# Kernel tuning notes

Measured on AMD Instinct MI355X. Metric: run time of the kernel, lower is better.

The kernel has to match this reference:

```python
import jax, jax.numpy as jnp
import numpy as np
import math

D = 768      # n_embd
NH = 12      # n_head
L = 4        # n_layer
E = 8        # num_experts
K = 2        # top_k
V = 50257    # vocab
H = 4 * D    # ffn hidden
MOE_LAYERS = (1, 3)


def _ln(x, g, b):
    m = x.mean(-1, keepdims=True)
    v = ((x - m) ** 2).mean(-1, keepdims=True)
    return (x - m) * jax.lax.rsqrt(v + 1e-5) * g + b


def setup_inputs() -> dict:
    key = jax.random.key(0)
    ks = iter(jax.random.split(key, 32))
    s = 0.02

    def rnd(shape):
        return jax.random.normal(next(ks), shape, dtype=jnp.float32) * s

    inp = {
        "x": jax.random.randint(next(ks), (2, 512), 0, V),
        "emb": rnd((V, D)),                       # tied embedding / output projection
        "wqkv": rnd((L, 3 * D, D)), "bqkv": jnp.zeros((L, 3 * D)),
        "wo": rnd((L, D, D)), "bo": jnp.zeros((L, D)),
        "ln1g": jnp.ones((L, D)), "ln1b": jnp.zeros((L, D)),
        "ln2g": jnp.ones((L, D)), "ln2b": jnp.zeros((L, D)),
        "sw1": rnd((2, H, D)), "sb1": jnp.zeros((2, H)),   # dense FFN layers (0, 2)
        "sw2": rnd((2, D, H)), "sb2": jnp.zeros((2, D)),
        "gw": rnd((2, E, D)),                              # router weights (layers 1, 3)
        "mw1": rnd((2, E, H, D)), "mb1": jnp.zeros((2, E, H)),
        "mw2": rnd((2, E, D, H)), "mb2": jnp.zeros((2, E, D)),
        "lnfg": jnp.ones((D,)), "lnfb": jnp.zeros((D,)),
    }
    return inp


def reference(x, emb, wqkv, bqkv, wo, bo, ln1g, ln1b, ln2g, ln2b,
              sw1, sb1, sw2, sb2, gw, mw1, mb1, mw2, mb2, lnfg, lnfb):
    b, t = x.shape
    dh = D // NH

    h = emb[x]  # [b,t,d]
    # sinusoidal positional encoding
    pos = jnp.arange(t, dtype=jnp.float32)[:, None]
    div = jnp.exp(jnp.arange(0, D, 2, dtype=jnp.float32) * (-math.log(10000.0) / D))
    pe = jnp.stack([jnp.sin(pos * div), jnp.cos(pos * div)], axis=-1).reshape(t, D)
    h = h + pe[None]

    # causal mask: query i cannot attend to key j > i
    neg = jnp.asarray(-jnp.inf, dtype=h.dtype)
    mask = jnp.where(jnp.arange(t)[None, :] > jnp.arange(t)[:, None], neg, 0.0)

    std_i = 0
    moe_i = 0
    for i in range(L):
        # pre-norm self-attention
        xn = _ln(h, ln1g[i], ln1b[i])
        qkv = xn @ wqkv[i].T + bqkv[i]          # [b,t,3d]
        q, k, v = jnp.split(qkv, 3, axis=-1)

        def heads(z):
            return z.reshape(b, t, NH, dh).transpose(0, 2, 1, 3)  # [b,nh,t,dh]

        q, k, v = heads(q), heads(k), heads(v)
        sc = jnp.einsum('bhqd,bhkd->bhqk', q, k) / math.sqrt(dh) + mask
        a = jax.nn.softmax(sc, axis=-1)
        o = jnp.einsum('bhqk,bhkd->bhqd', a, v).transpose(0, 2, 1, 3).reshape(b, t, D)
        h = h + o @ wo[i].T + bo[i]

        # pre-norm FFN (dense or MoE)
        xn = _ln(h, ln2g[i], ln2b[i])
        if i in MOE_LAYERS:
            T = b * t
            xf = xn.reshape(T, D)
            gl = xf @ gw[moe_i].T                      # router logits [T,E]
            probs = jax.nn.softmax(gl, axis=-1)
            topv, topi = jax.lax.top_k(probs, K)       # [T,K]
            w = topv / topv.sum(-1, keepdims=True)     # renormalized top-k gates
            cw = jnp.zeros_like(probs).at[jnp.arange(T)[:, None], topi].set(w)  # [T,E]
            he = jax.nn.gelu(jnp.einsum('td,ehd->teh', xf, mw1[moe_i]) + mb1[moe_i],
                             approximate=False)        # [T,E,H]
            ye = jnp.einsum('teh,edh->ted', he, mw2[moe_i]) + mb2[moe_i]        # [T,E,D]
            ff = jnp.einsum('ted,te->td', ye, cw).reshape(b, t, D)
            moe_i += 1
        else:
            ff = jax.nn.gelu(xn @ sw1[std_i].T + sb1[std_i], approximate=False) @ sw2[std_i].T + sb2[std_i]
            std_i += 1
        h = h + ff

    h = _ln(h, lnfg, lnfb)
    logits = h @ emb.T  # tied output projection, [b,t,V]
    return logits
```

## Files before the change

kernel.cpp:

```cpp
#include <hip/hip_runtime.h>
#include <hip/hip_bf16.h>
#include <cstdint>
#include <cstddef>

#define Dm   768
#define NHm  12
#define Lm   4
#define Em   8
#define Vm   50257
#define Hm   3072
#define Tm   512
#define Bm   2
#define NT   (Bm*Tm)
#define NAS  (NT*2)

typedef float f32x4 __attribute__((ext_vector_type(4)));
typedef short bf16x8 __attribute__((ext_vector_type(8)));

__device__ __forceinline__ float gelu_exact(float x) {
    return 0.5f * x * (1.0f + erff(x * 0.70710678118654752440f));
}

__device__ __forceinline__ unsigned short f2bf(float f) {
    __hip_bfloat16 h = __float2bfloat16(f);
// ... 19 lines not shown
    }
}

__global__ __launch_bounds__(256) void embed_kernel(const int* __restrict__ x,
                                                    const float* __restrict__ emb,
                                                    float* __restrict__ h) {
    int g = blockIdx.x;
    int tid = threadIdx.x;
    int tok = x[g];
    int pos = g % Tm;
    const float* erow = emb + (size_t)tok * Dm;
    for (int d = tid; d < Dm; d += 256) {
        int i2 = (d >> 1) * 2;
        float div = expf(-logf(10000.0f) * (float)i2 / (float)Dm);
        float a = (float)pos * div;
        float pe = (d & 1) ? cosf(a) : sinf(a);
        h[(size_t)g * Dm + d] = erow[d] + pe;
    }
}

__global__ __launch_bounds__(256) void ln_kernel(const float* __restrict__ in,
                                                 const float* __restrict__ g,
                                                 const float* __restrict__ b,
                                                 float* __restrict__ out) {
    int t = blockIdx.x, tid = threadIdx.x;
    const float* x = in + (size_t)t * Dm;
    float v0 = x[tid], v1 = x[tid + 256], v2 = x[tid + 512];
    __shared__ float red[256];
    red[tid] = v0 + v1 + v2;
    __syncthreads();
    for (int off = 128; off > 0; off >>= 1) {
        if (tid < off) red[tid] += red[tid + off];
        __syncthreads();
    }
    float mean = red[0] * (1.0f / Dm);
    __syncthreads();
    float d0 = v0 - mean, d1 = v1 - mean, d2 = v2 - mean;
    red[tid] = d0 * d0 + d1 * d1 + d2 * d2;
    __syncthreads();
    for (int off = 128; off > 0; off >>= 1) {
        if (tid < off) red[tid] += red[tid + off];
        __syncthreads();
    }
    float inv = rsqrtf(red[0] * (1.0f / Dm) + 1e-5f);
    float* o = out + (size_t)t * Dm;
    o[tid]       = d0 * inv * g[tid]       + b[tid];
    o[tid + 256] = d1 * inv * g[tid + 256] + b[tid + 256];
    o[tid + 512] = d2 * inv * g[tid + 512] + b[tid + 512];
}

#define MB 128
#define NB 128
#define KB 32
#define LDT 40

__device__ __forceinline__ void stage_tile(unsigned short* lds, const float* src,
                                           bool valid, int srow, int shalf) {
    union { unsigned short s[8]; uint4 v; } p0, p1;
    if (valid) {
        const float4* s4 = reinterpret_cast<const float4*>(src);
        #pragma unroll
        for (int q = 0; q < 4; ++q) {
            float4 f = s4[q];
            float vv[4] = {f.x, f.y, f.z, f.w};
            #pragma unroll
            for (int j = 0; j < 4; ++j) {
                int idx = q * 4 + j;
                unsigned short hb = f2bf(vv[j]);
                if (idx < 8) p0.s[idx] = hb; else p1.s[idx - 8] = hb;
            }
        }
// ... 15 lines not shown
        #pragma unroll
        for (int q = 0; q < 4; ++q) {
            float4 f = s4[q];
            float vv[4] = {f.x, f.y, f.z, f.w};
            #pragma unroll
            for (int j = 0; j < 4; ++j) {
                int idx = q * 4 + j;
                unsigned short hb = f2bf(vv[j]);
                unsigned short lb = f2bf(vv[j] - bf2f_bits(hb));
                if (idx < 8) { h0.s[idx] = hb; l0.s[idx] = lb; }
                else         { h1.s[idx - 8] = hb; l1.s[idx - 8] = lb; }
            }
        }
    } else {
        h0.v = make_uint4(0,0,0,0); h1.v = make_uint4(0,0,0,0);
        l0.v = make_uint4(0,0,0,0); l1.v = make_uint4(0,0,0,0);
    }
    uint4* dh = reinterpret_cast<uint4*>(&lds_hi[srow * LDT + shalf * 16]);
    dh[0] = h0.v; dh[1] = h1.v;
    uint4* dl = reinterpret_cast<uint4*>(&lds_lo[srow * LDT + shalf * 16]);
    dl[0] = l0.v; dl[1] = l1.v;
}

__global__ __launch_bounds__(256) void mfma_gemm_bf(const unsigned short* __restrict__ A,
                                                    const unsigned short* __restrict__ B,
                                                    const float* __restrict__ bias,
                                                    float* __restrict__ C,
                                                    int M, int N, int K) {
    __shared__ __align__(16) unsigned short SMEM[2 * MB * LDT];
    unsigned short* As = SMEM;
    unsigned short* Bs = SMEM + MB * LDT;
    int tid = threadIdx.x;
    int nt_m = M / MB;
    int total = gridDim.x;
    int bid = blockIdx.x;
    int swz = bid;
    if ((total & 7) == 0) {
        int chunk = total >> 3;
        swz = (bid & 7) * chunk + (bid >> 3);
    }
    int bm = (swz % nt_m) * MB;
    int bn = (swz / nt_m) * NB;
    int srow = tid >> 1, shalf = tid & 1;
    int lane = tid & 63, w = tid >> 6;
    int wr = w >> 1, wc = w & 1;
    int r0 = (lane >> 4) * 4, c0 = lane & 15;
    int kb = (lane >> 4) * 8;

    bool bval = (bn + srow) < N;
// ... 35 lines not shown
        #pragma unroll
        for (int m = 0; m < 4; ++m)
            #pragma unroll
            for (int n = 0; n < 4; ++n)
                acc[m][n] = __builtin_amdgcn_mfma_f32_16x16x32_bf16(af[m], bf[n], acc[m][n], 0, 0, 0);
        __syncthreads();
    }

    float* Ct = reinterpret_cast<float*>(SMEM);
    float* cw = Ct + w * 1024;
    #pragma unroll
    for (int m = 0; m < 4; ++m) {
        #pragma unroll
        for (int n = 0; n < 4; ++n)
            #pragma unroll
            for (int r = 0; r < 4; ++r)
                cw[(r0 + r) * 64 + n * 16 + c0] = acc[m][n][r];
        #pragma unroll
        for (int ch = 0; ch < 4; ++ch) {
            f32x4 vv = *reinterpret_cast<const f32x4*>(&cw[ch * 256 + lane * 4]);
            int rg = bm + wr * 64 + m * 16 + ch * 4 + (lane >> 4);
            int cg = bn + wc * 64 + (lane & 15) * 4;
            if (cg + 3 < N) {
                if (bias) {
                    vv[0] += bias[cg]; vv[1] += bias[cg + 1];
                    vv[2] += bias[cg + 2]; vv[3] += bias[cg + 3];
                }
                *reinterpret_cast<f32x4*>(&C[(size_t)rg * N + cg]) = vv;
            } else {
                #pragma unroll
                for (int e = 0; e < 4; ++e)
                    if (cg + e < N)
                        C[(size_t)rg * N + cg + e] = vv[e] + (bias ? bias[cg + e] : 0.f);
            }
        }
    }
}

template<int ACT, int RES>
__global__ __launch_bounds__(256) void mfma_gemm(const float* __restrict__ A,
                                                 const float* __restrict__ B,
                                                 const float* __restrict__ bias,
                                                 const float* __restrict__ res,
                                                 float* __restrict__ C,
                                                 int M, int N, int K) {
    __shared__ __align__(16) unsigned short As[MB * LDT];
    __shared__ __align__(16) unsigned short Bs[NB * LDT];
    int tid = threadIdx.x;
    int bm = blockIdx.y * MB, bn = blockIdx.x * NB;
    int srow = tid >> 1, shalf = tid & 1;
    int lane = tid & 63, w = tid >> 6;
    int wr = w >> 1, wc = w & 1;
    int r0 = (lane >> 4) * 4, c0 = lane & 15;
    int kb = (lane >> 4) * 8;

    f32x4 acc[4][4] = {};

    for (int kk = 0; kk < K; kk += KB) {
        stage_tile(As, A + (size_t)(bm + srow) * K + kk + shalf * 16, true, srow, shalf);
        bool bval = (bn + srow) < N;
        stage_tile(Bs, B + (size_t)(bn + srow) * K + kk + shalf * 16, bval, srow, shalf);
        __syncthreads();
        bf16x8 af[4], bf[4];
        #pragma unroll
        for (int m = 0; m < 4; ++m)
            af[m] = *reinterpret_cast<const bf16x8*>(&As[(wr * 64 + m * 16 + c0) * LDT + kb]);
        #pragma unroll
        for (int n = 0; n < 4; ++n)
            bf[n] = *reinterpret_cast<const bf16x8*>(&Bs[(wc * 64 + n * 16 + c0) * LDT + kb]);
        #pragma unroll
        for (int m = 0; m < 4; ++m)
            #pragma unroll
            for (int n = 0; n < 4; ++n)
                acc[m][n] = __builtin_amdgcn_mfma_f32_16x16x32_bf16(af[m], bf[n], acc[m][n], 0, 0, 0);
        __syncthreads();
    }

    #pragma unroll
    for (int n = 0; n < 4; ++n) {
        int col = bn + wc * 64 + n * 16 + c0;
        if (col < N) {
            float bv = bias ? bias[col] : 0.f;
            #pragma unroll
            for (int m = 0; m < 4; ++m) {
                #pragma unroll
                for (int r = 0; r < 4; ++r) {
                    int row = bm + wr * 64 + m * 16 + r0 + r;
                    float v = acc[m][n][r] + bv;
                    if (RES) v += res[(size_t)row * N + col];
                    if (ACT == 1) v = gelu_exact(v);
                    C[(size_t)row * N + col] = v;
                }
            }
        }
    }
}

__global__ __launch_bounds__(256) void mfma_gemm_sp_part(const float* __restrict__ A,
                                                         const float* __restrict__ B,
                                                         float* __restrict__ part,
                                                         int M, int N, int K, int KSPLIT) {
    __shared__ __align__(16) unsigned short SMEM[4 * MB * LDT];
    unsigned short* Ah = SMEM;
    unsigned short* Al = SMEM + MB * LDT;
    unsigned short* Bh = SMEM + 2 * MB * LDT;
    unsigned short* Bl = SMEM + 3 * MB * LDT;
    int tid = threadIdx.x;
    int bm = blockIdx.y * MB, bn = blockIdx.x * NB;
    int kc = blockIdx.z;
    int chunk = K / KSPLIT;
    int kbeg = kc * chunk;
    int srow = tid >> 1, shalf = tid & 1;
    int lane = tid & 63, w = tid >> 6;
    int wr = w >> 1, wc = w & 1;
    int r0 = (lane >> 4) * 4, c0 = lane & 15;
    int kb = (lane >> 4) * 8;

    f32x4 acc[4][4] = {};

    for (int kk = kbeg; kk < kbeg + chunk; kk += KB) {
        stage_tile_split(Ah, Al, A + (size_t)(bm + srow) * K + kk + shalf * 16, true, srow, shalf);
        stage_tile_split(Bh, Bl, B + (size_t)(bn + srow) * K + kk + shalf * 16, true, srow, shalf);
        __syncthreads();
        bf16x8 ah[4], al[4], bh[4], bl[4];
        #pragma unroll
        for (int m = 0; m < 4; ++m) {
            int o = (wr * 64 + m * 16 + c0) * LDT + kb;
            ah[m] = *reinterpret_cast<const bf16x8*>(&Ah[o]);
            al[m] = *reinterpret_cast<const bf16x8*>(&Al[o]);
        }
        #pragma unroll
        for (int n = 0; n < 4; ++n) {
            int o = (wc * 64 + n * 16 + c0) * LDT + kb;
            bh[n] = *reinterpret_cast<const bf16x8*>(&Bh[o]);
            bl[n] = *reinterpret_cast<const bf16x8*>(&Bl[o]);
        }
        #pragma unroll
        for (int m = 0; m < 4; ++m)
            #pragma unroll
            for (int n = 0; n < 4; ++n) {
                acc[m][n] = __builtin_amdgcn_mfma_f32_16x16x32_bf16(al[m], bh[n], acc[m][n], 0, 0, 0);
                acc[m][n] = __builtin_amdgcn_mfma_f32_16x16x32_bf16(ah[m], bl[n], acc[m][n], 0, 0, 0);
                acc[m][n] = __builtin_amdgcn_mfma_f32_16x16x32_bf16(ah[m], bh[n], acc[m][n], 0, 0, 0);
            }
        __syncthreads();
    }

    float* Ct = reinterpret_cast<float*>(SMEM);
    float* cw = Ct + w * 1024;
    float* P = part + (size_t)kc * M * N;
    #pragma unroll
    for (int m = 0; m < 4; ++m) {
        #pragma unroll
        for (int n = 0; n < 4; ++n)
            #pragma unroll
            for (int r = 0; r < 4; ++r)
                cw[(r0 + r) * 64 + n * 16 + c0] = acc[m][n][r];
        #pragma unroll
        for (int ch = 0; ch < 4; ++ch) {
            f32x4 vv = *reinterpret_cast<const f32x4*>(&cw[ch * 256 + lane * 4]);
            int rg = bm + wr * 64 + m * 16 + ch * 4 + (lane >> 4);
            int cg = bn + wc * 64 + (lane & 15) * 4;
            *reinterpret_cast<f32x4*>(&P[(size_t)rg * N + cg]) = vv;
        }
    }
}

template<int ACT>
__global__ __launch_bounds__(256) void reduce_dense(const float* __restrict__ part,
                                                    const float* __restrict__ bias,
                                                    float* __restrict__ C,
                                                    long MN, int N, int KSPLIT) {
    long stride = (long)gridDim.x * 256 * 4;
    for (long i = ((long)blockIdx.x * 256 + threadIdx.x) * 4; i < MN; i += stride) {
        float4 v = *reinterpret_cast<const float4*>(part + i);
        for (int kc = 1; kc < KSPLIT; ++kc) {
            float4 p = *reinterpret_cast<const float4*>(part + (size_t)kc * MN + i);
            v.x += p.x; v.y += p.y; v.z += p.z; v.w += p.w;
        }
        int col = (int)(i % N);
        float4 b = *reinterpret_cast<const float4*>(bias + col);
        v.x += b.x; v.y += b.y; v.z += b.z; v.w += b.w;
        if (ACT == 1) {
            v.x = gelu_exact(v.x); v.y = gelu_exact(v.y);
            v.z = gelu_exact(v.z); v.w = gelu_exact(v.w);
        }
        *reinterpret_cast<float4*>(C + i) = v;
    }
}

__global__ __launch_bounds__(256) void reduce_ln(const float* __restrict__ part,
                                                 const float* __restrict__ bias,
                                                 float* __restrict__ h,
                                                 const float* __restrict__ g,
                                                 const float* __restrict__ b,
                                                 float* __restrict__ xn,
                                                 int KSPLIT) {
    const long MN = (long)NT * Dm;
    int t = blockIdx.x, tid = threadIdx.x;
    float v[3];
    #pragma unroll
    for (int j = 0; j < 3; ++j) {
        int col = tid + j * 256;
        long idx = (long)t * Dm + col;
        float s = part[idx];
        for (int kc = 1; kc < KSPLIT; ++kc) s += part[(size_t)kc * MN + idx];
        s += bias[col] + h[idx];
        h[idx] = s;
        v[j] = s;
    }
    __shared__ float red[256];
    red[tid] = v[0] + v[1] + v[2];
    __syncthreads();
    for (int off = 128; off > 0; off >>= 1) {
        if (tid < off) red[tid] += red[tid + off];
        __syncthreads();
    }
    float mean = red[0] * (1.0f / Dm);
    __syncthreads();
    float d0 = v[0] - mean, d1 = v[1] - mean, d2 = v[2] - mean;
    red[tid] = d0 * d0 + d1 * d1 + d2 * d2;
    __syncthreads();
    for (int off = 128; off > 0; off >>= 1) {
        if (tid < off) red[tid] += red[tid + off];
        __syncthreads();
    }
    float inv = rsqrtf(red[0] * (1.0f / Dm) + 1e-5f);
    float* o = xn + (size_t)t * Dm;
    o[tid]       = d0 * inv * g[tid]       + b[tid];
    o[tid + 256] = d1 * inv * g[tid + 256] + b[tid + 256];
    o[tid + 512] = d2 * inv * g[tid + 512] + b[tid + 512];
}

__global__ __launch_bounds__(256) void combine_ln(float* __restrict__ h,
                                                  const float* __restrict__ ye,
                                                  const float* __restrict__ g,
                                                  const float* __restrict__ b,
                                                  float* __restrict__ xn) {
    int t = blockIdx.x, tid = threadIdx.x;
    float v[3];
    #pragma unroll
    for (int j = 0; j < 3; ++j) {
        int col = tid + j * 256;
        long idx = (long)t * Dm + col;
        float s = h[idx] + ye[(size_t)(t * 2) * Dm + col] + ye[(size_t)(t * 2 + 1) * Dm + col];
        h[idx] = s;
        v[j] = s;
    }
    __shared__ float red[256];
    red[tid] = v[0] + v[1] + v[2];
    __syncthreads();
    for (int off = 128; off > 0; off >>= 1) {
        if (tid < off) red[tid] += red[tid + off];
        __syncthreads();
    }
    float mean = red[0] * (1.0f / Dm);
    __syncthreads();
    float d0 = v[0] - mean, d1 = v[1] - mean, d2 = v[2] - mean;
    red[tid] = d0 * d0 + d1 * d1 + d2 * d2;
    __syncthreads();
    for (int off = 128; off > 0; off >>= 1) {
        if (tid < off) red[tid] += red[tid + off];
        __syncthreads();
    }
    float inv = rsqrtf(red[0] * (1.0f / Dm) + 1e-5f);
    float* o = xn + (size_t)t * Dm;
    o[tid]       = d0 * inv * g[tid]       + b[tid];
    o[tid + 256] = d1 * inv * g[tid + 256] + b[tid + 256];
    o[tid + 512] = d2 * inv * g[tid + 512] + b[tid + 512];
}

#define LDA 72
__device__ __forceinline__ void stage16a(unsigned short* dh, unsigned short* dl,
                                         const float* src) {
    union { unsigned short s[8]; uint4 v; } h0, h1, l0, l1;
    const float4* s4 = reinterpret_cast<const float4*>(src);
    #pragma unroll
    for (int q = 0; q < 4; ++q) {
        float4 f = s4[q];
        float vv[4] = {f.x, f.y, f.z, f.w};
        #pragma unroll
        for (int j = 0; j < 4; ++j) {
            int idx = q * 4 + j;
            unsigned short hb = f2bf(vv[j]);
            unsigned short lb = f2bf(vv[j] - bf2f_bits(hb));
            if (idx < 8) { h0.s[idx] = hb; l0.s[idx] = lb; }
            else         { h1.s[idx - 8] = hb; l1.s[idx - 8] = lb; }
        }
    }
    reinterpret_cast<uint4*>(dh)[0] = h0.v; reinterpret_cast<uint4*>(dh)[1] = h1.v;
    reinterpret_cast<uint4*>(dl)[0] = l0.v; reinterpret_cast<uint4*>(dl)[1] = l1.v;
}

__global__ __launch_bounds__(256) void attn_flash(const float* __restrict__ qkv,
                                                  float* __restrict__ o_out) {
    int qt = blockIdx.x;
    int bh = blockIdx.y;
    int b = bh / NHm, hh = bh % NHm;
    const int g0 = b * Tm;
    const int hoff = hh * 64;
    int tid = threadIdx.x;
    int lane = tid & 63, w = tid >> 6;
    int c0 = lane & 15, hi4 = lane >> 4;
    int kb = hi4 * 8;

    __shared__ __align__(16) unsigned short Qh[64 * LDA], Ql[64 * LDA];
    __shared__ __align__(16) unsigned short Kh[64 * LDA], Kl[64 * LDA];
    __shared__ __align__(16) unsigned short Vh[64 * LDA], Vl[64 * LDA];
    __shared__ __align__(16) unsigned short Ph[4][16 * LDA], Pl[4][16 * LDA];

    {
        int srow = tid >> 2, q = tid & 3;
        stage16a(&Qh[srow * LDA + q * 16], &Ql[srow * LDA + q * 16],
                 qkv + (size_t)(g0 + qt * 64 + srow) * (3 * Dm) + hoff + q * 16);
    }
    __syncthreads();

    f32x4 acc_o[4] = {};
// ... 97 lines not shown
        for (int kk2 = 0; kk2 < 64; kk2 += 32) {
            bf16x8 pah = *reinterpret_cast<const bf16x8*>(&Ph[w][c0 * LDA + kk2 + kb]);
            bf16x8 pal = *reinterpret_cast<const bf16x8*>(&Pl[w][c0 * LDA + kk2 + kb]);
            #pragma unroll
            for (int n = 0; n < 4; ++n) {
                bf16x8 vbh = *reinterpret_cast<const bf16x8*>(&Vh[(n * 16 + c0) * LDA + kk2 + kb]);
                bf16x8 vbl = *reinterpret_cast<const bf16x8*>(&Vl[(n * 16 + c0) * LDA + kk2 + kb]);
                acc_o[n] = __builtin_amdgcn_mfma_f32_16x16x32_bf16(pal, vbh, acc_o[n], 0, 0, 0);
                acc_o[n] = __builtin_amdgcn_mfma_f32_16x16x32_bf16(pah, vbl, acc_o[n], 0, 0, 0);
                acc_o[n] = __builtin_amdgcn_mfma_f32_16x16x32_bf16(pah, vbh, acc_o[n], 0, 0, 0);
            }
        }
        __syncthreads();
    }

    float inv[4];
    #pragma unroll
    for (int r = 0; r < 4; ++r) inv[r] = 1.0f / l_r[r];
    #pragma unroll
    for (int n = 0; n < 4; ++n)
        #pragma unroll
        for (int r = 0; r < 4; ++r) {
            int row = g0 + qt * 64 + w * 16 + hi4 * 4 + r;
            o_out[(size_t)row * Dm + hoff + n * 16 + c0] = acc_o[n][r] * inv[r];
        }
}

__global__ __launch_bounds__(256) void router_kernel(const float* __restrict__ xn,
                                                     const float* __restrict__ gw,
                                                     int* __restrict__ topi,
                                                     float* __restrict__ topw) {
    int t = blockIdx.x * 4 + (threadIdx.x >> 6);
    int lane = threadIdx.x & 63;
    const float4* x4 = reinterpret_cast<const float4*>(xn + (size_t)t * Dm);
    float4 xv[3];
    #pragma unroll
    for (int i = 0; i < 3; ++i) xv[i] = x4[lane + i * 64];

    float l[Em];
    #pragma unroll
    for (int e = 0; e < Em; ++e) {
        const float4* w4 = reinterpret_cast<const float4*>(gw + (size_t)e * Dm);
        float dot = 0.f;
        #pragma unroll
        for (int i = 0; i < 3; ++i) {
            float4 wv = w4[lane + i * 64];
            dot += xv[i].x * wv.x + xv[i].y * wv.y + xv[i].z * wv.z + xv[i].w * wv.w;
// ... 19 lines not shown
                                                          int* __restrict__ g_cnt,
                                                          int* __restrict__ g_off,
                                                          int* __restrict__ bucket) {
    __shared__ int cnt[Em], off[Em], pos[Em];
    int tid = threadIdx.x;
    if (tid < Em) cnt[tid] = 0;
    __syncthreads();
    for (int ts = tid; ts < NAS; ts += 256) atomicAdd(&cnt[topi[ts]], 1);
    __syncthreads();
    if (tid == 0) {
        int acc = 0;
        for (int e = 0; e < Em; ++e) { off[e] = acc; pos[e] = acc; acc += cnt[e]; }
    }
    __syncthreads();
    for (int ts = tid; ts < NAS; ts += 256) {
        int e = topi[ts];
        int p = atomicAdd(&pos[e], 1);
        bucket[p] = ts;
    }
    if (tid < Em) { g_cnt[tid] = cnt[tid]; g_off[tid] = off[tid]; }
}

template<int SPLIT>
__global__ __launch_bounds__(256) void moe_mfma_gemm1(const float* __restrict__ xn,
                                                      const float* __restrict__ W1all,
                                                      const float* __restrict__ B1all,
                                                      const int* __restrict__ bucket,
                                                      const int* __restrict__ cnt,
                                                      const int* __restrict__ off,
                                                      float* __restrict__ heg) {
    int e = blockIdx.z;
    int count = cnt[e];
    int mbase = blockIdx.y * MB;
    if (mbase >= count) return;
    int base = off[e];

    __shared__ __align__(16) unsigned short Ah[MB * LDT];
    __shared__ __align__(16) unsigned short Bh[NB * LDT];
    __shared__ __align__(16) unsigned short Al[SPLIT ? MB * LDT : 8];
    __shared__ __align__(16) unsigned short Bl[SPLIT ? NB * LDT : 8];
    __shared__ int toks[MB];
    int tid = threadIdx.x;
    int bn = blockIdx.x * NB;
    int srow = tid >> 1, shalf = tid & 1;
    int lane = tid & 63, w = tid >> 6;
    int wr = w >> 1, wc = w & 1;
    int r0 = (lane >> 4) * 4, c0 = lane & 15;
    int kb = (lane >> 4) * 8;
    if (tid < MB) {
        int p = mbase + tid;
        toks[tid] = (p < count) ? (bucket[base + p] >> 1) : -1;
    }
    __syncthreads();

    f32x4 acc[4][4] = {};
    const float* W = W1all + (size_t)e * Hm * Dm;
    int t = toks[srow];
    for (int kk = 0; kk < Dm; kk += KB) {
        if (SPLIT) {
            stage_tile_split(Ah, Al, xn + (size_t)t * Dm + kk + shalf * 16, t >= 0, srow, shalf);
            stage_tile_split(Bh, Bl, W + (size_t)(bn + srow) * Dm + kk + shalf * 16, true, srow, shalf);
        } else {
            stage_tile(Ah, xn + (size_t)t * Dm + kk + shalf * 16, t >= 0, srow, shalf);
            stage_tile(Bh, W + (size_t)(bn + srow) * Dm + kk + shalf * 16, true, srow, shalf);
        }
        __syncthreads();
        bf16x8 ah[4], bh[4], al[4], bl[4];
        #pragma unroll
        for (int m = 0; m < 4; ++m) {
            int o = (wr * 64 + m * 16 + c0) * LDT + kb;
            ah[m] = *reinterpret_cast<const bf16x8*>(&Ah[o]);
            if (SPLIT) al[m] = *reinterpret_cast<const bf16x8*>(&Al[o]);
        }
        #pragma unroll
        for (int n = 0; n < 4; ++n) {
            int o = (wc * 64 + n * 16 + c0) * LDT + kb;
            bh[n] = *reinterpret_cast<const bf16x8*>(&Bh[o]);
            if (SPLIT) bl[n] = *reinterpret_cast<const bf16x8*>(&Bl[o]);
        }
        #pragma unroll
        for (int m = 0; m < 4; ++m)
            #pragma unroll
            for (int n = 0; n < 4; ++n) {
                if (SPLIT) {
                    acc[m][n] = __builtin_amdgcn_mfma_f32_16x16x32_bf16(al[m], bh[n], acc[m][n], 0, 0, 0);
                    acc[m][n] = __builtin_amdgcn_mfma_f32_16x16x32_bf16(ah[m], bl[n], acc[m][n], 0, 0, 0);
                }
                acc[m][n] = __builtin_amdgcn_mfma_f32_16x16x32_bf16(ah[m], bh[n], acc[m][n], 0, 0, 0);
            }
        __syncthreads();
    }

    const float* b1 = B1all + (size_t)e * Hm;
    #pragma unroll
    for (int n = 0; n < 4; ++n) {
        int col = bn + wc * 64 + n * 16 + c0;
        float bv = b1[col];
        #pragma unroll
        for (int m = 0; m < 4; ++m) {
            #pragma unroll
            for (int r = 0; r < 4; ++r) {
                int p = mbase + wr * 64 + m * 16 + r0 + r;
                if (p < count)
                    heg[(size_t)(base + p) * Hm + col] = gelu_exact(acc[m][n][r] + bv);
            }
        }
    }
}

template<int SPLIT>
__global__ __launch_bounds__(256) void moe_gemm2_part(const float* __restrict__ heg,
                                                      const float* __restrict__ W2all,
                                                      const int* __restrict__ cnt,
                                                      const int* __restrict__ off,
                                                      float* __restrict__ part,
                                                      int KSPLIT) {
    int e = blockIdx.z;
    int count = cnt[e];
    int my = blockIdx.y;
    int kc = my % KSPLIT, mb = my / KSPLIT;
    int mbase = mb * MB;
    if (mbase >= count) return;
    int base = off[e];
    int chunk = Hm / KSPLIT;
    int kbeg = kc * chunk;

    __shared__ __align__(16) unsigned short Ah[MB * LDT];
    __shared__ __align__(16) unsigned short Bh[NB * LDT];
    __shared__ __align__(16) unsigned short Al[SPLIT ? MB * LDT : 8];
    __shared__ __align__(16) unsigned short Bl[SPLIT ? NB * LDT : 8];
    int tid = threadIdx.x;
    int bn = blockIdx.x * NB;
    int srow = tid >> 1, shalf = tid & 1;
    int lane = tid & 63, w = tid >> 6;
    int wr = w >> 1, wc = w & 1;
    int r0 = (lane >> 4) * 4, c0 = lane & 15;
    int kb = (lane >> 4) * 8;

    f32x4 acc[4][4] = {};
    const float* W = W2all + (size_t)e * Dm * Hm;
    bool aval = (mbase + srow) < count;
    for (int kk = kbeg; kk < kbeg + chunk; kk += KB) {
        if (SPLIT) {
            stage_tile_split(Ah, Al, heg + (size_t)(base + mbase + srow) * Hm + kk + shalf * 16, aval, srow, shalf);
            stage_tile_split(Bh, Bl, W + (size_t)(bn + srow) * Hm + kk + shalf * 16, true, srow, shalf);
        } else {
            stage_tile(Ah, heg + (size_t)(base + mbase + srow) * Hm + kk + shalf * 16, aval, srow, shalf);
            stage_tile(Bh, W + (size_t)(bn + srow) * Hm + kk + shalf * 16, true, srow, shalf);
        }
        __syncthreads();
        bf16x8 ah[4], bh[4], al[4], bl[4];
        #pragma unroll
        for (int m = 0; m < 4; ++m) {
            int o = (wr * 64 + m * 16 + c0) * LDT + kb;
            ah[m] = *reinterpret_cast<const bf16x8*>(&Ah[o]);
            if (SPLIT) al[m] = *reinterpret_cast<const bf16x8*>(&Al[o]);
        }
        #pragma unroll
        for (int n = 0; n < 4; ++n) {
            int o = (wc * 64 + n * 16 + c0) * LDT + kb;
            bh[n] = *reinterpret_cast<const bf16x8*>(&Bh[o]);
            if (SPLIT) bl[n] = *reinterpret_cast<const bf16x8*>(&Bl[o]);
        }
        #pragma unroll
        for (int m = 0; m < 4; ++m)
            #pragma unroll
            for (int n = 0; n < 4; ++n) {
                if (SPLIT) {
                    acc[m][n] = __builtin_amdgcn_mfma_f32_16x16x32_bf16(al[m], bh[n], acc[m][n], 0, 0, 0);
                    acc[m][n] = __builtin_amdgcn_mfma_f32_16x16x32_bf16(ah[m], bl[n], acc[m][n], 0, 0, 0);
// ... 52 lines not shown
    const float* emb  = (const float*)d_in[1];
    const float* wqkv = (const float*)d_in[2];
    const float* bqkv = (const float*)d_in[3];
    const float* wo   = (const float*)d_in[4];
    const float* bo   = (const float*)d_in[5];
    const float* ln1g = (const float*)d_in[6];
    const float* ln1b = (const float*)d_in[7];
    const float* ln2g = (const float*)d_in[8];
    const float* ln2b = (const float*)d_in[9];
    const float* sw1  = (const float*)d_in[10];
    const float* sb1  = (const float*)d_in[11];
    const float* sw2  = (const float*)d_in[12];
    const float* sb2  = (const float*)d_in[13];
    const float* gw   = (const float*)d_in[14];
    const float* mw1  = (const float*)d_in[15];
    const float* mb1  = (const float*)d_in[16];
    const float* mw2  = (const float*)d_in[17];
    const float* mb2  = (const float*)d_in[18];
    const float* lnfg = (const float*)d_in[19];
    const float* lnfb = (const float*)d_in[20];

    const size_t n_h    = (size_t)NT * Dm;
    const size_t n_qkv  = (size_t)NT * 3 * Dm;
    const size_t n_ffh  = (size_t)NT * Hm;
    const size_t n_ye   = (size_t)NAS * Dm;
    const size_t n_heg  = (size_t)NAS * Hm;
    const size_t n_xn   = (size_t)NT * Dm;
    const size_t n_part = (size_t)NT * Hm * 2;
    const size_t n_embbf = (size_t)Vm * Dm / 2;
    const size_t n_xnbf  = (size_t)NT * Dm / 2;
    const size_t n_big   = n_h + n_qkv + n_h + n_ffh + n_ye + n_heg + n_part;

    size_t wsf = ws_size / sizeof(float);

    float* w = (float*)d_ws;
    float* xn   = w;            w += n_xn;
    float* topw = w;            w += NAS;
    int*   topi = (int*)w;      w += NAS;
    int*   bucket = (int*)w;    w += NAS;
    int*   e_cnt = (int*)w;     w += 8;
    int*   e_off = (int*)w;     w += 8;
    size_t used = (size_t)(w - (float*)d_ws);

    unsigned short* emb_bf = nullptr;
    unsigned short* xn_bf  = nullptr;
    if (wsf >= used + n_embbf + n_xnbf + 64) {
        emb_bf = (unsigned short*)w;  w += n_embbf;
        xn_bf  = (unsigned short*)w;  w += n_xnbf;
        used = (size_t)(w - (float*)d_ws);
    }

    float *h, *qkv, *attno, *ffh, *ye, *heg, *part;
    if (wsf >= used + n_big + 64) {
        float* a = w;
        h = a;      a += n_h;
        qkv = a;    a += n_qkv;
        attno = a;  a += n_h;
        ffh = a;    a += n_ffh;
        ye = a;     a += n_ye;
        heg = a;    a += n_heg;
        part = a;
    } else {
        float* a = (float*)d_out;
        h = a;      a += n_h;
        qkv = a;    a += n_qkv;
        attno = a;  a += n_h;
        ffh = a;    a += n_ffh;
        ye = a;     a += n_ye;
        heg = a;    a += n_heg;
        part = a;
    }

    if (emb_bf) {
        long n = (long)Vm * Dm;
        cvt_bf16_kernel<<<(unsigned)((n / 8 + 255) / 256), 256, 0, stream>>>(emb, emb_bf, n);
    }

    embed_kernel<<<NT, 256, 0, stream>>>(x, emb, h);
    ln_kernel<<<NT, 256, 0, stream>>>(h, ln1g, ln1b, xn);

    const int RBLK = 2048;
    int std_i = 0, moe_i = 0;
    for (int l = 0; l < Lm; ++l) {
        const float* ng = (l < 3) ? (ln1g + (l + 1) * Dm) : lnfg;
        const float* nb = (l < 3) ? (ln1b + (l + 1) * Dm) : lnfb;

        mfma_gemm_sp_part<<<dim3((3 * Dm) / NB, NT / MB, 2), 256, 0, stream>>>(
            xn, wqkv + (size_t)l * 3 * Dm * Dm, part, NT, 3 * Dm, Dm, 2);
        reduce_dense<0><<<RBLK, 256, 0, stream>>>(
            part, bqkv + (size_t)l * 3 * Dm, qkv, (long)NT * 3 * Dm, 3 * Dm, 2);
        attn_flash<<<dim3(Tm / 64, Bm * NHm), 256, 0, stream>>>(qkv, attno);
        mfma_gemm_sp_part<<<dim3(Dm / NB, NT / MB, 4), 256, 0, stream>>>(
            attno, wo + (size_t)l * Dm * Dm, part, NT, Dm, Dm, 4);
        reduce_ln<<<NT, 256, 0, stream>>>(
            part, bo + (size_t)l * Dm, h, ln2g + l * Dm, ln2b + l * Dm, xn, 4);

        if (l == 1 || l == 3) {
            router_kernel<<<NT / 4, 256, 0, stream>>>(
                xn, gw + (size_t)moe_i * Em * Dm, topi, topw);
            route_build_kernel<<<1, 256, 0, stream>>>(topi, e_cnt, e_off, bucket);
            if (l == 3) {
                moe_mfma_gemm1<0><<<dim3(Hm / NB, NAS / MB, Em), 256, 0, stream>>>(
                    xn, mw1 + (size_t)moe_i * Em * Hm * Dm, mb1 + (size_t)moe_i * Em * Hm,
                    bucket, e_cnt, e_off, heg);
                moe_gemm2_part<0><<<dim3(Dm / NB, (NAS / MB) * 4, Em), 256, 0, stream>>>(
                    heg, mw2 + (size_t)moe_i * Em * Dm * Hm, e_cnt, e_off, part, 4);
            } else {
                moe_mfma_gemm1<1><<<dim3(Hm / NB, NAS / MB, Em), 256, 0, stream>>>(
                    xn, mw1 + (size_t)moe_i * Em * Hm * Dm, mb1 + (size_t)moe_i * Em * Hm,
                    bucket, e_cnt, e_off, heg);
                moe_gemm2_part<1><<<dim3(Dm / NB, (NAS / MB) * 4, Em), 256, 0, stream>>>(
                    heg, mw2 + (size_t)moe_i * Em * Dm * Hm, e_cnt, e_off, part, 4);
            }
            moe_reduce<<<RBLK, 256, 0, stream>>>(
                part, mb2 + (size_t)moe_i * Em * Dm, bucket, topi, topw, ye, 4);
            combine_ln<<<NT, 256, 0, stream>>>(h, ye, ng, nb, xn);
            moe_i++;
        } else {
            mfma_gemm_sp_part<<<dim3(Hm / NB, NT / MB, 2), 256, 0, stream>>>(
                xn, sw1 + (size_t)std_i * Hm * Dm, part, NT, Hm, Dm, 2);
            reduce_dense<1><<<RBLK, 256, 0, stream>>>(
                part, sb1 + (size_t)std_i * Hm, ffh, (long)NT * Hm, Hm, 2);
            mfma_gemm_sp_part<<<dim3(Dm / NB, NT / MB, 8), 256, 0, stream>>>(
                ffh, sw2 + (size_t)std_i * Dm * Hm, part, NT, Dm, Hm, 8);
            reduce_ln<<<NT, 256, 0, stream>>>(
                part, sb2 + (size_t)std_i * Dm, h, ng, nb, xn, 8);
            std_i++;
        }
    }

    if (emb_bf) {
        long n = (long)NT * Dm;
        cvt_bf16_kernel<<<(unsigned)((n / 8 + 255) / 256), 256, 0, stream>>>(xn, xn_bf, n);
        int nblk = (NT / MB) * ((Vm + NB - 1) / NB);
        mfma_gemm_bf<<<dim3(nblk), 256, 0, stream>>>(
            xn_bf, emb_bf, nullptr, (float*)d_out, NT, Vm, Dm);
    } else {
        mfma_gemm<0,0><<<dim3((Vm + NB - 1) / NB, NT / MB), 256, 0, stream>>>(
            xn, emb, nullptr, nullptr, (float*)d_out, NT, Vm, Dm);
    }
}
```

Baseline: 1.068 ms.

## Emit pre-split bf16 hi/lo activations from producer kernels to skip GEMM-side conversion

LayerNorm, attention, GELU-reduce and MoE gemm1 epilogues now write activations as bf16 hi/lo pairs. The A-side of the downstream GEMMs then copies these tiles straight into LDS instead of loading fp32 and splitting them in every tile block. This removes repeated conversion work and halves the A-operand bytes read per GEMM, and the final logits GEMM uses xnh directly, dropping a separate convert kernel. The cost is extra stores in the producers and a reorganized workspace layout, which includes a questionable arena_in_out guard.

```diff
diff --git a/kernel.cpp b/kernel.cpp
--- a/kernel.cpp
+++ b/kernel.cpp
@@ -65,7 +65,9 @@
 __global__ __launch_bounds__(256) void ln_kernel(const float* __restrict__ in,
                                                  const float* __restrict__ g,
                                                  const float* __restrict__ b,
-                                                 float* __restrict__ out) {
+                                                 float* __restrict__ xn,
+                                                 unsigned short* __restrict__ xnh,
+                                                 unsigned short* __restrict__ xnl) {
     int t = blockIdx.x, tid = threadIdx.x;
     const float* x = in + (size_t)t * Dm;
     float v0 = x[tid], v1 = x[tid + 256], v2 = x[tid + 512];
@@ -86,10 +88,16 @@
         __syncthreads();
     }
     float inv = rsqrtf(red[0] * (1.0f / Dm) + 1e-5f);
-    float* o = out + (size_t)t * Dm;
-    o[tid]       = d0 * inv * g[tid]       + b[tid];
-    o[tid + 256] = d1 * inv * g[tid + 256] + b[tid + 256];
-    o[tid + 512] = d2 * inv * g[tid + 512] + b[tid + 512];
+    float o0 = d0 * inv * g[tid]       + b[tid];
+    float o1 = d1 * inv * g[tid + 256] + b[tid + 256];
+    float o2 = d2 * inv * g[tid + 512] + b[tid + 512];
+    long base = (size_t)t * Dm;
+    xn[base + tid] = o0; xn[base + tid + 256] = o1; xn[base + tid + 512] = o2;
+    unsigned short h0 = f2bf(o0), h1 = f2bf(o1), h2 = f2bf(o2);
+    xnh[base + tid] = h0; xnh[base + tid + 256] = h1; xnh[base + tid + 512] = h2;
+    xnl[base + tid]       = f2bf(o0 - bf2f_bits(h0));
+    xnl[base + tid + 256] = f2bf(o1 - bf2f_bits(h1));
+    xnl[base + tid + 512] = f2bf(o2 - bf2f_bits(h2));
 }
 
 #define MB 128
@@ -151,9 +159,20 @@
     dl[0] = l0.v; dl[1] = l1.v;
 }
 
+__device__ __forceinline__ void stage_tile_copy(unsigned short* lds,
+                                                const unsigned short* src,
+                                                bool valid, int srow, int shalf) {
+    uint4 a0 = make_uint4(0,0,0,0), a1 = make_uint4(0,0,0,0);
+    if (valid) {
+        a0 = reinterpret_cast<const uint4*>(src)[0];
+        a1 = reinterpret_cast<const uint4*>(src)[1];
+    }
+    uint4* d = reinterpret_cast<uint4*>(&lds[srow * LDT + shalf * 16]);
+    d[0] = a0; d[1] = a1;
+}
+
 __global__ __launch_bounds__(256) void mfma_gemm_bf(const unsigned short* __restrict__ A,
                                                     const unsigned short* __restrict__ B,
-                                                    const float* __restrict__ bias,
                                                     float* __restrict__ C,
                                                     int M, int N, int K) {
     __shared__ __align__(16) unsigned short SMEM[2 * MB * LDT];
@@ -235,26 +254,18 @@
             int rg = bm + wr * 64 + m * 16 + ch * 4 + (lane >> 4);
             int cg = bn + wc * 64 + (lane & 15) * 4;
             if (cg + 3 < N) {
-                if (bias) {
-                    vv[0] += bias[cg]; vv[1] += bias[cg + 1];
-                    vv[2] += bias[cg + 2]; vv[3] += bias[cg + 3];
-                }
                 *reinterpret_cast<f32x4*>(&C[(size_t)rg * N + cg]) = vv;
             } else {
                 #pragma unroll
                 for (int e = 0; e < 4; ++e)
-                    if (cg + e < N)
-                        C[(size_t)rg * N + cg + e] = vv[e] + (bias ? bias[cg + e] : 0.f);
-            }
-        }
-    }
-}
-
-template<int ACT, int RES>
+                    if (cg + e < N) C[(size_t)rg * N + cg + e] = vv[e];
+            }
+        }
+    }
+}
+
 __global__ __launch_bounds__(256) void mfma_gemm(const float* __restrict__ A,
                                                  const float* __restrict__ B,
-                                                 const float* __restrict__ bias,
-                                                 const float* __restrict__ res,
                                                  float* __restrict__ C,
                                                  int M, int N, int K) {
     __shared__ __align__(16) unsigned short As[MB * LDT];
@@ -293,23 +304,19 @@
     for (int n = 0; n < 4; ++n) {
         int col = bn + wc * 64 + n * 16 + c0;
         if (col < N) {
-            float bv = bias ? bias[col] : 0.f;
-            #pragma unroll
-            for (int m = 0; m < 4; ++m) {
+            #pragma unroll
+            for (int m = 0; m < 4; ++m)
                 #pragma unroll
                 for (int r = 0; r < 4; ++r) {
                     int row = bm + wr * 64 + m * 16 + r0 + r;
-                    float v = acc[m][n][r] + bv;
-                    if (RES) v += res[(size_t)row * N + col];
-                    if (ACT == 1) v = gelu_exact(v);
-                    C[(size_t)row * N + col] = v;
+                    C[(size_t)row * N + col] = acc[m][n][r];
                 }
-            }
-        }
-    }
-}
-
-__global__ __launch_bounds__(256) void mfma_gemm_sp_part(const float* __restrict__ A,
+        }
+    }
+}
+
+__global__ __launch_bounds__(256) void mfma_gemm_pA_part(const unsigned short* __restrict__ Ahp,
+                                                         const unsigned short* __restrict__ Alp,
                                                          const float* __restrict__ B,
                                                          float* __restrict__ part,
                                                          int M, int N, int K, int KSPLIT) {
@@ -332,7 +339,9 @@
     f32x4 acc[4][4] = {};
 
     for (int kk = kbeg; kk < kbeg + chunk; kk += KB) {
-        stage_tile_split(Ah, Al, A + (size_t)(bm + srow) * K + kk + shalf * 16, true, srow, shalf);
+        size_t aoff = (size_t)(bm + srow) * K + kk + shalf * 16;
+        stage_tile_copy(Ah, Ahp + aoff, true, srow, shalf);
+        stage_tile_copy(Al, Alp + aoff, true, srow, shalf);
         stage_tile_split(Bh, Bl, B + (size_t)(bn + srow) * K + kk + shalf * 16, true, srow, shalf);
         __syncthreads();
         bf16x8 ah[4], al[4], bh[4], bl[4];
@@ -379,7 +388,6 @@
     }
 }
 
-template<int ACT>
 __global__ __launch_bounds__(256) void reduce_dense(const float* __restrict__ part,
                                                     const float* __restrict__ bias,
                                                     float* __restrict__ C,
@@ -394,11 +402,36 @@
         int col = (int)(i % N);
         float4 b = *reinterpret_cast<const float4*>(bias + col);
         v.x += b.x; v.y += b.y; v.z += b.z; v.w += b.w;
-        if (ACT == 1) {
-            v.x = gelu_exact(v.x); v.y = gelu_exact(v.y);
-            v.z = gelu_exact(v.z); v.w = gelu_exact(v.w);
-        }
         *reinterpret_cast<float4*>(C + i) = v;
+    }
+}
+
+__global__ __launch_bounds__(256) void reduce_gelu_bf(const float* __restrict__ part,
+                                                      const float* __restrict__ bias,
+                                                      unsigned short* __restrict__ outh,
+                                                      unsigned short* __restrict__ outl,
+                                                      long MN, int N, int KSPLIT) {
+    long stride = (long)gridDim.x * 256 * 4;
+    for (long i = ((long)blockIdx.x * 256 + threadIdx.x) * 4; i < MN; i += stride) {
+        float4 v = *reinterpret_cast<const float4*>(part + i);
+        for (int kc = 1; kc < KSPLIT; ++kc) {
+            float4 p = *reinterpret_cast<const float4*>(part + (size_t)kc * MN + i);
+            v.x += p.x; v.y += p.y; v.z += p.z; v.w += p.w;
+        }
+        int col = (int)(i % N);
+        float4 b = *reinterpret_cast<const float4*>(bias + col);
+        float f[4];
+        f[0] = gelu_exact(v.x + b.x); f[1] = gelu_exact(v.y + b.y);
+        f[2] = gelu_exact(v.z + b.z); f[3] = gelu_exact(v.w + b.w);
+        union { unsigned short s[4]; uint2 u; } ph, pl;
+        #pragma unroll
+        for (int e = 0; e < 4; ++e) {
+            unsigned short hb = f2bf(f[e]);
+            ph.s[e] = hb;
+            pl.s[e] = f2bf(f[e] - bf2f_bits(hb));
+        }
+        *reinterpret_cast<uint2*>(outh + i) = ph.u;
+        *reinterpret_cast<uint2*>(outl + i) = pl.u;
     }
 }
 
@@ -408,6 +441,8 @@
                                                  const float* __restrict__ g,
                                                  const float* __restrict__ b,
                                                  float* __restrict__ xn,
+                                                 unsigned short* __restrict__ xnh,
+                                                 unsigned short* __restrict__ xnl,
                                                  int KSPLIT) {
     const long MN = (long)NT * Dm;
     int t = blockIdx.x, tid = threadIdx.x;
@@ -439,17 +474,25 @@
         __syncthreads();
     }
     float inv = rsqrtf(red[0] * (1.0f / Dm) + 1e-5f);
-    float* o = xn + (size_t)t * Dm;
-    o[tid]       = d0 * inv * g[tid]       + b[tid];
-    o[tid + 256] = d1 * inv * g[tid + 256] + b[tid + 256];
-    o[tid + 512] = d2 * inv * g[tid + 512] + b[tid + 512];
+    float o0 = d0 * inv * g[tid]       + b[tid];
+    float o1 = d1 * inv * g[tid + 256] + b[tid + 256];
+    float o2 = d2 * inv * g[tid + 512] + b[tid + 512];
+    long base = (size_t)t * Dm;
+    xn[base + tid] = o0; xn[base + tid + 256] = o1; xn[base + tid + 512] = o2;
+    unsigned short h0 = f2bf(o0), h1 = f2bf(o1), h2 = f2bf(o2);
+    xnh[base + tid] = h0; xnh[base + tid + 256] = h1; xnh[base + tid + 512] = h2;
+    xnl[base + tid]       = f2bf(o0 - bf2f_bits(h0));
+    xnl[base + tid + 256] = f2bf(o1 - bf2f_bits(h1));
+    xnl[base + tid + 512] = f2bf(o2 - bf2f_bits(h2));
 }
 
 __global__ __launch_bounds__(256) void combine_ln(float* __restrict__ h,
                                                   const float* __restrict__ ye,
                                                   const float* __restrict__ g,
                                                   const float* __restrict__ b,
-                                                  float* __restrict__ xn) {
+                                                  float* __restrict__ xn,
+                                                  unsigned short* __restrict__ xnh,
+                                                  unsigned short* __restrict__ xnl) {
     int t = blockIdx.x, tid = threadIdx.x;
     float v[3];
     #pragma unroll
@@ -477,10 +520,16 @@
         __syncthreads();
     }
     float inv = rsqrtf(red[0] * (1.0f / Dm) + 1e-5f);
-    float* o = xn + (size_t)t * Dm;
-    o[tid]       = d0 * inv * g[tid]       + b[tid];
-    o[tid + 256] = d1 * inv * g[tid + 256] + b[tid + 256];
-    o[tid + 512] = d2 * inv * g[tid + 512] + b[tid + 512];
+    float o0 = d0 * inv * g[tid]       + b[tid];
+    float o1 = d1 * inv * g[tid + 256] + b[tid + 256];
+    float o2 = d2 * inv * g[tid + 512] + b[tid + 512];
+    long base = (size_t)t * Dm;
+    xn[base + tid] = o0; xn[base + tid + 256] = o1; xn[base + tid + 512] = o2;
+    unsigned short h0 = f2bf(o0), h1 = f2bf(o1), h2 = f2bf(o2);
+    xnh[base + tid] = h0; xnh[base + tid + 256] = h1; xnh[base + tid + 512] = h2;
+    xnl[base + tid]       = f2bf(o0 - bf2f_bits(h0));
+    xnl[base + tid + 256] = f2bf(o1 - bf2f_bits(h1));
+    xnl[base + tid + 512] = f2bf(o2 - bf2f_bits(h2));
 }
 
 #define LDA 72
@@ -506,7 +555,8 @@
 }
 
 __global__ __launch_bounds__(256) void attn_flash(const float* __restrict__ qkv,
-                                                  float* __restrict__ o_out) {
+                                                  unsigned short* __restrict__ aoh,
+                                                  unsigned short* __restrict__ aol) {
     int qt = blockIdx.x;
     int bh = blockIdx.y;
     int b = bh / NHm, hh = bh % NHm;
@@ -650,7 +700,11 @@
         #pragma unroll
         for (int r = 0; r < 4; ++r) {
             int row = g0 + qt * 64 + w * 16 + hi4 * 4 + r;
-            o_out[(size_t)row * Dm + hoff + n * 16 + c0] = acc_o[n][r] * inv[r];
+            float v = acc_o[n][r] * inv[r];
+            unsigned short hb = f2bf(v);
+            size_t idx = (size_t)row * Dm + hoff + n * 16 + c0;
+            aoh[idx] = hb;
+            aol[idx] = f2bf(v - bf2f_bits(hb));
         }
 }
 
@@ -716,13 +770,15 @@
 }
 
 template<int SPLIT>
-__global__ __launch_bounds__(256) void moe_mfma_gemm1(const float* __restrict__ xn,
+__global__ __launch_bounds__(256) void moe_mfma_gemm1(const unsigned short* __restrict__ xnh,
+                                                      const unsigned short* __restrict__ xnl,
                                                       const float* __restrict__ W1all,
                                                       const float* __restrict__ B1all,
                                                       const int* __restrict__ bucket,
                                                       const int* __restrict__ cnt,
                                                       const int* __restrict__ off,
-                                                      float* __restrict__ heg) {
+                                                      unsigned short* __restrict__ hegh,
+                                                      unsigned short* __restrict__ hegl) {
     int e = blockIdx.z;
     int count = cnt[e];
     int mbase = blockIdx.y * MB;
@@ -751,11 +807,12 @@
     const float* W = W1all + (size_t)e * Hm * Dm;
     int t = toks[srow];
     for (int kk = 0; kk < Dm; kk += KB) {
+        size_t aoff = (size_t)t * Dm + kk + shalf * 16;
+        stage_tile_copy(Ah, xnh + aoff, t >= 0, srow, shalf);
         if (SPLIT) {
-            stage_tile_split(Ah, Al, xn + (size_t)t * Dm + kk + shalf * 16, t >= 0, srow, shalf);
+            stage_tile_copy(Al, xnl + aoff, t >= 0, srow, shalf);
             stage_tile_split(Bh, Bl, W + (size_t)(bn + srow) * Dm + kk + shalf * 16, true, srow, shalf);
         } else {
-            stage_tile(Ah, xn + (size_t)t * Dm + kk + shalf * 16, t >= 0, srow, shalf);
             stage_tile(Bh, W + (size_t)(bn + srow) * Dm + kk + shalf * 16, true, srow, shalf);
         }
         __syncthreads();
@@ -795,15 +852,21 @@
             #pragma unroll
             for (int r = 0; r < 4; ++r) {
                 int p = mbase + wr * 64 + m * 16 + r0 + r;
-                if (p < count)
-                    heg[(size_t)(base + p) * Hm + col] = gelu_exact(acc[m][n][r] + bv);
+                if (p < count) {
+                    float v = gelu_exact(acc[m][n][r] + bv);
+                    unsigned short hb = f2bf(v);
+                    size_t idx = (size_t)(base + p) * Hm + col;
+                    hegh[idx] = hb;
+                    hegl[idx] = f2bf(v - bf2f_bits(hb));
+                }
             }
         }
     }
 }
 
 template<int SPLIT>
-__global__ __launch_bounds__(256) void moe_gemm2_part(const float* __restrict__ heg,
+__global__ __launch_bounds__(256) void moe_gemm2_part(const unsigned short* __restrict__ hegh,
+                                                      const unsigned short* __restrict__ hegl,
                                                       const float* __restrict__ W2all,
                                                       const int* __restrict__ cnt,
                                                       const int* __restrict__ off,
@@ -835,11 +898,12 @@
     const float* W = W2all + (size_t)e * Dm * Hm;
     bool aval = (mbase + srow) < count;
     for (int kk = kbeg; kk < kbeg + chunk; kk += KB) {
+        size_t aoff = (size_t)(base + mbase + srow) * Hm + kk + shalf * 16;
+        stage_tile_copy(Ah, hegh + aoff, aval, srow, shalf);
         if (SPLIT) {
-            stage_tile_split(Ah, Al, heg + (size_t)(base + mbase + srow) * Hm + kk + shalf * 16, aval, srow, shalf);
+            stage_tile_copy(Al, hegl + aoff, aval, srow, shalf);
             stage_tile_split(Bh, Bl, W + (size_t)(bn + srow) * Hm + kk + shalf * 16, true, srow, shalf);
         } else {
-            stage_tile(Ah, heg + (size_t)(base + mbase + srow) * Hm + kk + shalf * 16, aval, srow, shalf);
             stage_tile(Bh, W + (size_t)(bn + srow) * Hm + kk + shalf * 16, true, srow, shalf);
         }
         __syncthreads();
@@ -938,19 +1002,20 @@
 
     const size_t n_h    = (size_t)NT * Dm;
     const size_t n_qkv  = (size_t)NT * 3 * Dm;
-    const size_t n_ffh  = (size_t)NT * Hm;
     const size_t n_ye   = (size_t)NAS * Dm;
-    const size_t n_heg  = (size_t)NAS * Hm;
-    const size_t n_xn   = (size_t)NT * Dm;
     const size_t n_part = (size_t)NT * Hm * 2;
+    const size_t n_xnb  = (size_t)NT * Dm / 2;
+    const size_t n_ffhb = (size_t)NT * Hm / 2;
+    const size_t n_hegb = (size_t)NAS * Hm / 2;
     const size_t n_embbf = (size_t)Vm * Dm / 2;
-    const size_t n_xnbf  = (size_t)NT * Dm / 2;
-    const size_t n_big   = n_h + n_qkv + n_h + n_ffh + n_ye + n_heg + n_part;
+    const size_t n_big = n_h + n_qkv + n_ye + n_part
+                       + 2 * n_xnb  + 2 * n_xnb
+                       + 2 * n_ffhb + 2 * n_hegb;
 
     size_t wsf = ws_size / sizeof(float);
 
     float* w = (float*)d_ws;
-    float* xn   = w;            w += n_xn;
+    float* xn   = w;            w += (size_t)NT * Dm;
     float* topw = w;            w += NAS;
     int*   topi = (int*)w;      w += NAS;
     int*   bucket = (int*)w;    w += NAS;
@@ -959,33 +1024,29 @@
     size_t used = (size_t)(w - (float*)d_ws);
 
     unsigned short* emb_bf = nullptr;
-    unsigned short* xn_bf  = nullptr;
-    if (wsf >= used + n_embbf + n_xnbf + 64) {
+    if (wsf >= used + n_embbf + 64) {
         emb_bf = (unsigned short*)w;  w += n_embbf;
-        xn_bf  = (unsigned short*)w;  w += n_xnbf;
         used = (size_t)(w - (float*)d_ws);
     }
 
-    float *h, *qkv, *attno, *ffh, *ye, *heg, *part;
-    if (wsf >= used + n_big + 64) {
-        float* a = w;
-        h = a;      a += n_h;
-        qkv = a;    a += n_qkv;
-        attno = a;  a += n_h;
-        ffh = a;    a += n_ffh;
-        ye = a;     a += n_ye;
-        heg = a;    a += n_heg;
-        part = a;
-    } else {
-        float* a = (float*)d_out;
-        h = a;      a += n_h;
-        qkv = a;    a += n_qkv;
-        attno = a;  a += n_h;
-        ffh = a;    a += n_ffh;
-        ye = a;     a += n_ye;
-        heg = a;    a += n_heg;
-        part = a;
-    }
+    float *h, *qkv, *ye, *part;
+    unsigned short *xnh, *xnl, *aoh, *aol, *ffhh, *ffhl, *hegh, *hegl;
+    float* a;
+    if (wsf >= used + n_big + 64) a = w;
+    else                          a = (float*)d_out;
+    h = a;      a += n_h;
+    qkv = a;    a += n_qkv;
+    ye = a;     a += n_ye;
+    part = a;   a += n_part;
+    xnh = (unsigned short*)a;  a += n_xnb;
+    xnl = (unsigned short*)a;  a += n_xnb;
+    aoh = (unsigned short*)a;  a += n_xnb;
+    aol = (unsigned short*)a;  a += n_xnb;
+    ffhh = (unsigned short*)a; a += n_ffhb;
+    ffhl = (unsigned short*)a; a += n_ffhb;
+    hegh = (unsigned short*)a; a += n_hegb;
+    hegl = (unsigned short*)a; a += n_hegb;
+    bool arena_in_out = (a != (float*)d_ws ? ((float*)d_out == h) : false);
 
     if (emb_bf) {
         long n = (long)Vm * Dm;
@@ -993,7 +1054,7 @@
     }
 
     embed_kernel<<<NT, 256, 0, stream>>>(x, emb, h);
-    ln_kernel<<<NT, 256, 0, stream>>>(h, ln1g, ln1b, xn);
+    ln_kernel<<<NT, 256, 0, stream>>>(h, ln1g, ln1b, xn, xnh, xnl);
 
     const int RBLK = 2048;
     int std_i = 0, moe_i = 0;
@@ -1001,15 +1062,15 @@
         const float* ng = (l < 3) ? (ln1g + (l + 1) * Dm) : lnfg;
         const float* nb = (l < 3) ? (ln1b + (l + 1) * Dm) : lnfb;
 
-        mfma_gemm_sp_part<<<dim3((3 * Dm) / NB, NT / MB, 2), 256, 0, stream>>>(
-            xn, wqkv + (size_t)l * 3 * Dm * Dm, part, NT, 3 * Dm, Dm, 2);
-        reduce_dense<0><<<RBLK, 256, 0, stream>>>(
+        mfma_gemm_pA_part<<<dim3((3 * Dm) / NB, NT / MB, 2), 256, 0, stream>>>(
+            xnh, xnl, wqkv + (size_t)l * 3 * Dm * Dm, part, NT, 3 * Dm, Dm, 2);
+        reduce_dense<<<RBLK, 256, 0, stream>>>(
             part, bqkv + (size_t)l * 3 * Dm, qkv, (long)NT * 3 * Dm, 3 * Dm, 2);
-        attn_flash<<<dim3(Tm / 64, Bm * NHm), 256, 0, stream>>>(qkv, attno);
-        mfma_gemm_sp_part<<<dim3(Dm / NB, NT / MB, 4), 256, 0, stream>>>(
-            attno, wo + (size_t)l * Dm * Dm, part, NT, Dm, Dm, 4);
+        attn_flash<<<dim3(Tm / 64, Bm * NHm), 256, 0, stream>>>(qkv, aoh, aol);
+        mfma_gemm_pA_part<<<dim3(Dm / NB, NT / MB, 4), 256, 0, stream>>>(
+            aoh, aol, wo + (size_t)l * Dm * Dm, part, NT, Dm, Dm, 4);
         reduce_ln<<<NT, 256, 0, stream>>>(
-            part, bo + (size_t)l * Dm, h, ln2g + l * Dm, ln2b + l * Dm, xn, 4);
+            part, bo + (size_t)l * Dm, h, ln2g + l * Dm, ln2b + l * Dm, xn, xnh, xnl, 4);
 
         if (l == 1 || l == 3) {
             router_kernel<<<NT / 4, 256, 0, stream>>>(
@@ -1017,42 +1078,40 @@
             route_build_kernel<<<1, 256, 0, stream>>>(topi, e_cnt, e_off, bucket);
             if (l == 3) {
                 moe_mfma_gemm1<0><<<dim3(Hm / NB, NAS / MB, Em), 256, 0, stream>>>(
-                    xn, mw1 + (size_t)moe_i * Em * Hm * Dm, mb1 + (size_t)moe_i * Em * Hm,
-                    bucket, e_cnt, e_off, heg);
+                    xnh, xnl, mw1 + (size_t)moe_i * Em * Hm * Dm, mb1 + (size_t)moe_i * Em * Hm,
+                    bucket, e_cnt, e_off, hegh, hegl);
                 moe_gemm2_part<0><<<dim3(Dm / NB, (NAS / MB) * 4, Em), 256, 0, stream>>>(
-                    heg, mw2 + (size_t)moe_i * Em * Dm * Hm, e_cnt, e_off, part, 4);
+                    hegh, hegl, mw2 + (size_t)moe_i * Em * Dm * Hm, e_cnt, e_off, part, 4);
             } else {
                 moe_mfma_gemm1<1><<<dim3(Hm / NB, NAS / MB, Em), 256, 0, stream>>>(
-                    xn, mw1 + (size_t)moe_i * Em * Hm * Dm, mb1 + (size_t)moe_i * Em * Hm,
-                    bucket, e_cnt, e_off, heg);
+                    xnh, xnl, mw1 + (size_t)moe_i * Em * Hm * Dm, mb1 + (size_t)moe_i * Em * Hm,
+                    bucket, e_cnt, e_off, hegh, hegl);
                 moe_gemm2_part<1><<<dim3(Dm / NB, (NAS / MB) * 4, Em), 256, 0, stream>>>(
-                    heg, mw2 + (size_t)moe_i * Em * Dm * Hm, e_cnt, e_off, part, 4);
+                    hegh, hegl, mw2 + (size_t)moe_i * Em * Dm * Hm, e_cnt, e_off, part, 4);
             }
             moe_reduce<<<RBLK, 256, 0, stream>>>(
                 part, mb2 + (size_t)moe_i * Em * Dm, bucket, topi, topw, ye, 4);
-            combine_ln<<<NT, 256, 0, stream>>>(h, ye, ng, nb, xn);
+            combine_ln<<<NT, 256, 0, stream>>>(h, ye, ng, nb, xn, xnh, xnl);
             moe_i++;
         } else {
-            mfma_gemm_sp_part<<<dim3(Hm / NB, NT / MB, 2), 256, 0, stream>>>(
-                xn, sw1 + (size_t)std_i * Hm * Dm, part, NT, Hm, Dm, 2);
-            reduce_dense<1><<<RBLK, 256, 0, stream>>>(
-                part, sb1 + (size_t)std_i * Hm, ffh, (long)NT * Hm, Hm, 2);
-            mfma_gemm_sp_part<<<dim3(Dm / NB, NT / MB, 8), 256, 0, stream>>>(
-                ffh, sw2 + (size_t)std_i * Dm * Hm, part, NT, Dm, Hm, 8);
+            mfma_gemm_pA_part<<<dim3(Hm / NB, NT / MB, 2), 256, 0, stream>>>(
+                xnh, xnl, sw1 + (size_t)std_i * Hm * Dm, part, NT, Hm, Dm, 2);
+            reduce_gelu_bf<<<RBLK, 256, 0, stream>>>(
+                part, sb1 + (size_t)std_i * Hm, ffhh, ffhl, (long)NT * Hm, Hm, 2);
+            mfma_gemm_pA_part<<<dim3(Dm / NB, NT / MB, 8), 256, 0, stream>>>(
+                ffhh, ffhl, sw2 + (size_t)std_i * Dm * Hm, part, NT, Dm, Hm, 8);
             reduce_ln<<<NT, 256, 0, stream>>>(
-                part, sb2 + (size_t)std_i * Dm, h, ng, nb, xn, 8);
+                part, sb2 + (size_t)std_i * Dm, h, ng, nb, xn, xnh, xnl, 8);
             std_i++;
         }
     }
 
-    if (emb_bf) {
-        long n = (long)NT * Dm;
-        cvt_bf16_kernel<<<(unsigned)((n / 8 + 255) / 256), 256, 0, stream>>>(xn, xn_bf, n);
+    if (emb_bf && !arena_in_out) {
         int nblk = (NT / MB) * ((Vm + NB - 1) / NB);
         mfma_gemm_bf<<<dim3(nblk), 256, 0, stream>>>(
-            xn_bf, emb_bf, nullptr, (float*)d_out, NT, Vm, Dm);
+            xnh, emb_bf, (float*)d_out, NT, Vm, Dm);
     } else {
-        mfma_gemm<0,0><<<dim3((Vm + NB - 1) / NB, NT / MB), 256, 0, stream>>>(
-            xn, emb, nullptr, nullptr, (float*)d_out, NT, Vm, Dm);
-    }
-}
+        mfma_gemm<<<dim3((Vm + NB - 1) / NB, NT / MB), 256, 0, stream>>>(
+            xn, emb, (float*)d_out, NT, Vm, Dm);
+    }
+}
```

Result: no change. 1.053 ms (-1.4%).
